# Kernel tuning notes

Measured on AMD Instinct MI355X. Metric: run time of the kernel, lower is better.

The kernel has to match this reference:

```python
import jax, jax.numpy as jnp
import numpy as np
from jax import lax

# Dimensions (see shape_source)
B, J, I, E, H = 256, 128, 64, 512, 512   # batch, target len, source len, embed, hidden
MAXJW = 128                               # max jump width
WJ = 2 * MAXJW + 1                        # size of jump-width set (257)
ALPHA_P0 = 1.0
EPS = 1e-29


def setup_inputs() -> dict:
    key = jax.random.key(0)
    ks = jax.random.split(key, 10)
    return {
        "y_hidden": jax.random.normal(ks[0], (B, J, E), jnp.float32),
        "y_hidden_null": jax.random.normal(ks[1], (1, 1, E), jnp.float32),
        "W_trans": jax.random.normal(ks[2], (E, H), jnp.float32) * 0.02,
        "b_trans": jnp.zeros((H,), jnp.float32),
        "W_jump": jax.random.normal(ks[3], (H, WJ), jnp.float32) * 0.02,
        "b_jump": jnp.zeros((WJ,), jnp.float32),
        "W_p0": jax.random.normal(ks[4], (H, 1), jnp.float32) * 0.02,
        "b_p0": jnp.zeros((1,), jnp.float32),
        # emission probs p(source_t | target_state_k), kept near 1 to avoid
        # underflow of the unrescaled HMM forward product (as in original).
        "emission": jax.random.uniform(ks[5], (B, 2 * J, I), jnp.float32) * 0.5 + 0.75,
        "source_lengths": jax.random.randint(ks[6], (B,), 1, I + 1, dtype=jnp.int32),
        "target_lengths": jax.random.randint(ks[7], (B,), 1, J + 1, dtype=jnp.int32),
    }


def _build_transition(y_hidden, y_hidden_null, W_trans, b_trans, W_jump, b_jump, W_p0, b_p0):
    # get_transition: Dense(tanh) -> Dense(softmax) jump widths; Dense(sigmoid) p0.
    ts = jnp.tanh(y_hidden @ W_trans + b_trans)           # [B,J,H]
    ts_null = jnp.tanh(y_hidden_null @ W_trans + b_trans) # [1,1,H]
    jump_prob = jax.nn.softmax(ts @ W_jump + b_jump, axis=-1)  # [B,J,WJ]
    p0_scalar = ALPHA_P0 * jax.nn.sigmoid(ts_null @ W_p0 + b_p0)[0, 0, 0]
    p0 = jnp.broadcast_to(p0_scalar, (y_hidden.shape[0], J))  # tile to [B,J]
    # gather jump widths: row i takes jump_prob[:, i, MAXJW + k - i] for k in [0,J)
    idx = MAXJW + jnp.arange(J)[None, :] - jnp.arange(J)[:, None]        # [J,J]
    idxb = jnp.broadcast_to(idx[None], (jump_prob.shape[0], J, J))
    jw = jnp.take_along_axis(jump_prob, idxb, axis=2)                    # [B,J,J]
    jw = jw * (1.0 - p0[:, :, None]) / jnp.sum(jw, axis=2, keepdims=True)
    diag_p0 = p0[:, :, None] * jnp.eye(J, dtype=jw.dtype)                # [B,J,J]
    T_half = jnp.concatenate([jw, diag_p0], axis=2)                      # [B,J,2J]
    return jnp.concatenate([T_half, T_half], axis=1)                     # [B,2J,2J]


def reference(y_hidden, y_hidden_null, W_trans, b_trans, W_jump, b_jump,
              W_p0, b_p0, emission, source_lengths, target_lengths):
    T = _build_transition(y_hidden, y_hidden_null, W_trans, b_trans,
                          W_jump, b_jump, W_p0, b_p0)       # [B,2J,2J]
    e = jnp.transpose(emission, (2, 0, 1))                  # [I,B,2J]
    # tf.scan with no initializer: f_0 = emission at source position 0
    f0 = e[0]

    def step(f, et):
        f_next = jnp.einsum('bj,bjk->bk', f, T) * et        # forward recursion
        return f_next, f_next

    _, fs = lax.scan(step, f0, e[1:])
    fs = jnp.concatenate([f0[None], fs], axis=0)            # [I,B,2J]
    fbt = jnp.transpose(fs, (1, 2, 0))                      # [B,2J,I]
    last_idx = (source_lengths - 1).astype(jnp.int32)[:, None, None]
    last = jnp.take_along_axis(fbt, last_idx, axis=2)[:, :, 0]  # [B,2J]
    m = (jnp.arange(J)[None, :] < target_lengths[:, None]).astype(last.dtype)
    mask = jnp.concatenate([m, m], axis=1)                  # [B,2J]
    return jnp.log(jnp.sum(last * mask, axis=1) + EPS)      # [B]
```

## Files before the change

kernel.cpp:

```cpp
#include <hip/hip_runtime.h>
#include <stdint.h>

typedef __attribute__((ext_vector_type(8))) short bf16x8;
typedef __attribute__((ext_vector_type(4))) float f32x4;

__device__ __forceinline__ unsigned short f2bf(float f) {
  union { float f; unsigned int u; } un; un.f = f;
  unsigned int r = un.u + 0x7fffu + ((un.u >> 16) & 1u);
  return (unsigned short)(r >> 16);
}

__device__ __forceinline__ float tanh_fast(float x) {
  x = fminf(15.f, fmaxf(-15.f, x));
  float e = __expf(2.f * x);
  return (e - 1.f) / (e + 1.f);
}

__device__ __forceinline__ void gload_lds16(const void* g, void* l) {
  __builtin_amdgcn_global_load_lds(
      (const __attribute__((address_space(1))) unsigned int*)(unsigned long long)g,
      (__attribute__((address_space(3))) unsigned int*)(unsigned int)(unsigned long long)l,
      16, 0, 0);
}

__global__ __launch_bounds__(256) void cvt_y_kernel(
    const float* __restrict__ x, unsigned short* __restrict__ y, int n4) {
  int i = blockIdx.x * blockDim.x + threadIdx.x;
  if (i < n4) {
    const float4 v = reinterpret_cast<const float4*>(x)[i];
    ushort4 o;
    o.x = f2bf(v.x); o.y = f2bf(v.y); o.z = f2bf(v.z); o.w = f2bf(v.w);
    reinterpret_cast<ushort4*>(y)[i] = o;
  }
}

__global__ __launch_bounds__(256) void cvt_transpose_kernel(
    const float* __restrict__ W, unsigned short* __restrict__ Wt,
    int R, int C, int ldW) {
  int i = blockIdx.x * blockDim.x + threadIdx.x;
  if (i < R * C) {
    int c = i / R, r = i - c * R;
    Wt[(size_t)c * R + r] = f2bf(W[(size_t)r * ldW + c]);
  }
}

__global__ __launch_bounds__(512) void p0_kernel(
    const float* __restrict__ ynull, const float* __restrict__ W_trans,
    const float* __restrict__ b_trans, const float* __restrict__ W_p0,
    const float* __restrict__ b_p0, float* __restrict__ p0buf) {
  __shared__ float red[512];
  const int hh = threadIdx.x;
  float acc = 0.f;
  for (int e = 0; e < 512; ++e) acc = fmaf(ynull[e], W_trans[(size_t)e * 512 + hh], acc);
  const float ts = tanhf(acc + b_trans[hh]);
  red[hh] = ts * W_p0[hh];
  __syncthreads();
  for (int s = 256; s > 0; s >>= 1) {
    if (hh < s) red[hh] += red[hh + s];
    __syncthreads();
  }
  if (hh == 0) {
    const float z = red[0] + b_p0[0];
    const float p0 = 1.f / (1.f + __expf(-z));
    p0buf[0] = p0;
    p0buf[1] = 1.f - p0;
  }
}

template <int EPI>
__global__ __launch_bounds__(256, 2) void gemm_tt(
    const unsigned short* __restrict__ A, const unsigned short* __restrict__ Bt,
    const float* __restrict__ bias, void* __restrict__ Cout,
    int M, int N, int K) {
  __shared__ unsigned short sA[128 * 32];
  __shared__ unsigned short sB[128 * 32];
  const int tid = threadIdx.x;
  const int lane = tid & 63;
  const int wave = tid >> 6;
  const int wr = wave >> 1, wc = wave & 1;
  const int m0 = blockIdx.x * 128, n0 = blockIdx.y * 128;

  f32x4 acc[4][4] = {};

  const int srow = lane >> 2;
  const int scol = (lane & 3) * 8;
  const int c0 = wave * 2, c1 = wave * 2 + 1;
  const unsigned short* Ar0 = A + (size_t)(m0 + c0 * 16 + srow) * K + scol;
  const unsigned short* Ar1 = A + (size_t)(m0 + c1 * 16 + srow) * K + scol;
  const unsigned short* Br0 = Bt + (size_t)(n0 + c0 * 16 + srow) * K + scol;
  const unsigned short* Br1 = Bt + (size_t)(n0 + c1 * 16 + srow) * K + scol;

  for (int kk = 0; kk < K; kk += 32) {
    __syncthreads();
    gload_lds16(Ar0 + kk, &sA[c0 * 512]);
    gload_lds16(Ar1 + kk, &sA[c1 * 512]);
    gload_lds16(Br0 + kk, &sB[c0 * 512]);
    gload_lds16(Br1 + kk, &sB[c1 * 512]);
    __syncthreads();
    bf16x8 af[4], bfr[4];
#pragma unroll
    for (int mi = 0; mi < 4; ++mi)
      af[mi] = *reinterpret_cast<const bf16x8*>(
          &sA[(wr * 64 + mi * 16 + (lane & 15)) * 32 + (lane >> 4) * 8]);
#pragma unroll
    for (int ni = 0; ni < 4; ++ni)
      bfr[ni] = *reinterpret_cast<const bf16x8*>(
          &sB[(wc * 64 + ni * 16 + (lane & 15)) * 32 + (lane >> 4) * 8]);
#pragma unroll
    for (int mi = 0; mi < 4; ++mi)
#pragma unroll
      for (int ni = 0; ni < 4; ++ni)
        acc[mi][ni] = __builtin_amdgcn_mfma_f32_16x16x32_bf16(
            af[mi], bfr[ni], acc[mi][ni], 0, 0, 0);
  }

  const int crow0 = m0 + wr * 64 + (lane >> 4) * 4;
  const int ccol0 = n0 + wc * 64 + (lane & 15);
#pragma unroll
  for (int mi = 0; mi < 4; ++mi) {
#pragma unroll
    for (int ni = 0; ni < 4; ++ni) {
      const int gcol = ccol0 + ni * 16;
      const float bv = bias[gcol];
#pragma unroll
      for (int r = 0; r < 4; ++r) {
        const int grow = crow0 + mi * 16 + r;
        const float v = acc[mi][ni][r] + bv;
        if constexpr (EPI == 0) {
          ((unsigned short*)Cout)[(size_t)grow * N + gcol] = f2bf(tanh_fast(v));
        } else {
          ((float*)Cout)[(size_t)grow * N + gcol] = v;
        }
      }
    }
  }
}

__global__ __launch_bounds__(256) void wsoftmax_kernel(
    const float* __restrict__ logits, const float* __restrict__ p0buf,
    float* __restrict__ jwout) {
  const int lane = threadIdx.x & 63;
  const int wave = threadIdx.x >> 6;
  const int row = blockIdx.x * 4 + wave;
  const int i = row & 127;
  const float* lrow = logits + (size_t)row * 256 + (128 - i);
  const float v0 = lrow[lane];
  const float v1 = lrow[lane + 64];
  float mx = fmaxf(v0, v1);
#pragma unroll
  for (int off = 32; off > 0; off >>= 1) mx = fmaxf(mx, __shfl_xor(mx, off));
  const float e0 = __expf(v0 - mx);
  const float e1 = __expf(v1 - mx);
  float s = e0 + e1;
#pragma unroll
  for (int off = 32; off > 0; off >>= 1) s += __shfl_xor(s, off);
  const float scale = p0buf[1] / s;
  float* orow = jwout + (size_t)row * 128;
  orow[lane] = e0 * scale;
  orow[lane + 64] = e1 * scale;
}

__global__ __launch_bounds__(256, 1) void forward_hmm(
    const float* __restrict__ jw, const float* __restrict__ emission,
    const float* __restrict__ p0buf, const int* __restrict__ slen_p,
    const int* __restrict__ tlen_p, float* __restrict__ out) {
  __shared__ float gbuf[2][128];
  __shared__ float part[2][128];
  __shared__ float red[4];
  const int b = blockIdx.x;
  const int tid = threadIdx.x;
  const int k = tid & 127;
  const int h = tid >> 7;
  const int lane = tid & 63;
  const int wave = tid >> 6;

  const float* eb = emission + (size_t)b * 256 * 64;

  float jwreg[64];
  {
    const float* jb = jw + (size_t)b * 16384 + (size_t)(h * 64) * 128 + k;
#pragma unroll
    for (int j = 0; j < 64; ++j) jwreg[j] = jb[(size_t)j * 128];
  }
  const float p0 = p0buf[0];
  const int S = slen_p[b];
  const int T = tlen_p[b];

  if (h == 0) gbuf[0][k] = eb[k * 64] + eb[(128 + k) * 64];
  __syncthreads();

  const int steps = S - 1;
  int cur = 0;
  for (int t = 1; t <= steps; ++t) {
    float e0 = 0.f, e1 = 0.f;
    if (h == 0) {
      e0 = eb[k * 64 + t];
      e1 = eb[(128 + k) * 64 + t];
    }
    float acc = 0.f;
    const float* gv = &gbuf[cur][h * 64];
#pragma unroll
    for (int c = 0; c < 16; ++c) {
      const float4 g4 = *reinterpret_cast<const float4*>(&gv[c * 4]);
      acc = fmaf(g4.x, jwreg[c * 4 + 0], acc);
      acc = fmaf(g4.y, jwreg[c * 4 + 1], acc);
      acc = fmaf(g4.z, jwreg[c * 4 + 2], acc);
      acc = fmaf(g4.w, jwreg[c * 4 + 3], acc);
    }
    part[h][k] = acc;
    __syncthreads();
    if (h == 0) {
      const float s = part[0][k] + part[1][k];
      gbuf[cur ^ 1][k] = fmaf(s, e0, gbuf[cur][k] * p0 * e1);
    }
    __syncthreads();
    cur ^= 1;
  }

  float val = 0.f;
  if (h == 0 && k < T) val = gbuf[cur][k];
#pragma unroll
  for (int off = 32; off > 0; off >>= 1) val += __shfl_xor(val, off);
  if (lane == 0) red[wave] = val;
  __syncthreads();
  if (tid == 0) out[b] = logf(red[0] + red[1] + red[2] + red[3] + 1e-29f);
}

extern "C" void kernel_launch(void* const* d_in, const int* in_sizes, int n_in,
                              void* d_out, int out_size, void* d_ws, size_t ws_size,
                              hipStream_t stream) {
  const float* y_hidden = (const float*)d_in[0];
  const float* y_null   = (const float*)d_in[1];
  const float* W_trans  = (const float*)d_in[2];
  const float* b_trans  = (const float*)d_in[3];
  const float* W_jump   = (const float*)d_in[4];
  const float* b_jump   = (const float*)d_in[5];
  const float* W_p0     = (const float*)d_in[6];
  const float* b_p0     = (const float*)d_in[7];
  const float* emission = (const float*)d_in[8];
  const int* slen = (const int*)d_in[9];
  const int* tlen = (const int*)d_in[10];
  float* out = (float*)d_out;

  char* ws = (char*)d_ws;
  unsigned short* a16   = (unsigned short*)ws;
  float* logits         = (float*)ws;
  unsigned short* ts16  = (unsigned short*)(ws + 33554432);
  unsigned short* wt16t = (unsigned short*)(ws + 67108864);
  unsigned short* wj16t = (unsigned short*)(ws + 67633152);
  float* p0buf          = (float*)(ws + 67895296);
  float* jwbuf          = (float*)(ws + 67895552);

  cvt_y_kernel<<<dim3(16384), dim3(256), 0, stream>>>(y_hidden, a16, 16777216 / 4);
  cvt_transpose_kernel<<<dim3((512 * 512 + 255) / 256), dim3(256), 0, stream>>>(
      W_trans, wt16t, 512, 512, 512);
  cvt_transpose_kernel<<<dim3((512 * 256 + 255) / 256), dim3(256), 0, stream>>>(
      W_jump, wj16t, 512, 256, 257);
  p0_kernel<<<dim3(1), dim3(512), 0, stream>>>(y_null, W_trans, b_trans, W_p0, b_p0, p0buf);

  gemm_tt<0><<<dim3(256, 4), dim3(256), 0, stream>>>(a16, wt16t, b_trans, (void*)ts16,
                                                     32768, 512, 512);
  gemm_tt<1><<<dim3(256, 2), dim3(256), 0, stream>>>(ts16, wj16t, b_jump, (void*)logits,
                                                     32768, 256, 512);
  wsoftmax_kernel<<<dim3(8192), dim3(256), 0, stream>>>(logits, p0buf, jwbuf);
  forward_hmm<<<dim3(256), dim3(256), 0, stream>>>(jwbuf, emission, p0buf, slen, tlen, out);
}
```

Baseline: 135.7 us.

## Run HMM forward recursion on MFMA with bf16 transition in a single wave

```diff
diff --git a/kernel.cpp b/kernel.cpp
--- a/kernel.cpp
+++ b/kernel.cpp
@@ -14,6 +14,12 @@
   x = fminf(15.f, fmaxf(-15.f, x));
   float e = __expf(2.f * x);
   return (e - 1.f) / (e + 1.f);
+}
+
+__device__ __forceinline__ unsigned int cvt_pk_bf16(float lo, float hi) {
+  unsigned int r;
+  asm("v_cvt_pk_bf16_f32 %0, %1, %2" : "=v"(r) : "v"(lo), "v"(hi));
+  return r;
 }
 
 __device__ __forceinline__ void gload_lds16(const void* g, void* l) {
@@ -138,7 +144,7 @@
 
 __global__ __launch_bounds__(256) void wsoftmax_kernel(
     const float* __restrict__ logits, const float* __restrict__ p0buf,
-    float* __restrict__ jwout) {
+    unsigned short* __restrict__ jwout) {
   const int lane = threadIdx.x & 63;
   const int wave = threadIdx.x >> 6;
   const int row = blockIdx.x * 4 + wave;
@@ -155,75 +161,98 @@
 #pragma unroll
   for (int off = 32; off > 0; off >>= 1) s += __shfl_xor(s, off);
   const float scale = p0buf[1] / s;
-  float* orow = jwout + (size_t)row * 128;
-  orow[lane] = e0 * scale;
-  orow[lane + 64] = e1 * scale;
-}
-
-__global__ __launch_bounds__(256, 1) void forward_hmm(
-    const float* __restrict__ jw, const float* __restrict__ emission,
+  unsigned short* orow = jwout + (size_t)row * 128;
+  orow[lane] = f2bf(e0 * scale);
+  orow[lane + 64] = f2bf(e1 * scale);
+}
+
+__global__ __launch_bounds__(64, 1) void forward_hmm_mfma(
+    const unsigned short* __restrict__ jwb,
+    const float* __restrict__ emission,
     const float* __restrict__ p0buf, const int* __restrict__ slen_p,
     const int* __restrict__ tlen_p, float* __restrict__ out) {
-  __shared__ float gbuf[2][128];
-  __shared__ float part[2][128];
-  __shared__ float red[4];
+  __shared__ float gl[128];
   const int b = blockIdx.x;
-  const int tid = threadIdx.x;
-  const int k = tid & 127;
-  const int h = tid >> 7;
-  const int lane = tid & 63;
-  const int wave = tid >> 6;
-
-  const float* eb = emission + (size_t)b * 256 * 64;
-
-  float jwreg[64];
-  {
-    const float* jb = jw + (size_t)b * 16384 + (size_t)(h * 64) * 128 + k;
-#pragma unroll
-    for (int j = 0; j < 64; ++j) jwreg[j] = jb[(size_t)j * 128];
-  }
+  const int l = threadIdx.x;
+  const int m = l & 15;
+  const int q = l >> 4;
+
+  const unsigned short* jwt = jwb + (size_t)b * 16384;
+  bf16x8 bfr[4][8];
+#pragma unroll
+  for (int kt = 0; kt < 4; ++kt) {
+    const int r0 = kt * 32 + q * 8;
+#pragma unroll
+    for (int nt = 0; nt < 8; ++nt) {
+      const int c = nt * 16 + m;
+      bf16x8 v;
+#pragma unroll
+      for (int j = 0; j < 8; ++j) v[j] = (short)jwt[(size_t)(r0 + j) * 128 + c];
+      bfr[kt][nt] = v;
+    }
+  }
+
   const float p0 = p0buf[0];
   const int S = slen_p[b];
   const int T = tlen_p[b];
-
-  if (h == 0) gbuf[0][k] = eb[k * 64] + eb[(128 + k) * 64];
-  __syncthreads();
-
-  const int steps = S - 1;
-  int cur = 0;
-  for (int t = 1; t <= steps; ++t) {
-    float e0 = 0.f, e1 = 0.f;
-    if (h == 0) {
-      e0 = eb[k * 64 + t];
-      e1 = eb[(128 + k) * 64 + t];
-    }
-    float acc = 0.f;
-    const float* gv = &gbuf[cur][h * 64];
-#pragma unroll
-    for (int c = 0; c < 16; ++c) {
-      const float4 g4 = *reinterpret_cast<const float4*>(&gv[c * 4]);
-      acc = fmaf(g4.x, jwreg[c * 4 + 0], acc);
-      acc = fmaf(g4.y, jwreg[c * 4 + 1], acc);
-      acc = fmaf(g4.z, jwreg[c * 4 + 2], acc);
-      acc = fmaf(g4.w, jwreg[c * 4 + 3], acc);
-    }
-    part[h][k] = acc;
-    __syncthreads();
-    if (h == 0) {
-      const float s = part[0][k] + part[1][k];
-      gbuf[cur ^ 1][k] = fmaf(s, e0, gbuf[cur][k] * p0 * e1);
-    }
-    __syncthreads();
-    cur ^= 1;
+  const float* eb = emission + (size_t)b * 16384;
+
+  float gown[8];
+#pragma unroll
+  for (int nt = 0; nt < 8; ++nt) {
+    const int k = nt * 16 + m;
+    gown[nt] = eb[(size_t)k * 64] + eb[(size_t)(k + 128) * 64];
+  }
+  if (q == 0) {
+#pragma unroll
+    for (int nt = 0; nt < 8; ++nt) gl[nt * 16 + m] = gown[nt];
+  }
+
+  for (int t = 1; t < S; ++t) {
+    float e0[8], e1[8];
+#pragma unroll
+    for (int nt = 0; nt < 8; ++nt) {
+      const int k = nt * 16 + m;
+      e0[nt] = eb[(size_t)k * 64 + t];
+      e1[nt] = eb[(size_t)(k + 128) * 64 + t];
+    }
+    bf16x8 af[4];
+#pragma unroll
+    for (int kt = 0; kt < 4; ++kt) {
+      const float4 lo = *reinterpret_cast<const float4*>(&gl[kt * 32 + q * 8]);
+      const float4 hi = *reinterpret_cast<const float4*>(&gl[kt * 32 + q * 8 + 4]);
+      union { unsigned int u[4]; bf16x8 v; } pk;
+      pk.u[0] = cvt_pk_bf16(lo.x, lo.y);
+      pk.u[1] = cvt_pk_bf16(lo.z, lo.w);
+      pk.u[2] = cvt_pk_bf16(hi.x, hi.y);
+      pk.u[3] = cvt_pk_bf16(hi.z, hi.w);
+      af[kt] = pk.v;
+    }
+    f32x4 acc[8];
+#pragma unroll
+    for (int nt = 0; nt < 8; ++nt) {
+      f32x4 a = __builtin_amdgcn_mfma_f32_16x16x32_bf16(
+          af[0], bfr[0][nt], (f32x4){0.f, 0.f, 0.f, 0.f}, 0, 0, 0);
+      a = __builtin_amdgcn_mfma_f32_16x16x32_bf16(af[1], bfr[1][nt], a, 0, 0, 0);
+      a = __builtin_amdgcn_mfma_f32_16x16x32_bf16(af[2], bfr[2][nt], a, 0, 0, 0);
+      acc[nt] = __builtin_amdgcn_mfma_f32_16x16x32_bf16(af[3], bfr[3][nt], a, 0, 0, 0);
+    }
+#pragma unroll
+    for (int nt = 0; nt < 8; ++nt)
+      gown[nt] = fmaf(acc[nt][0], e0[nt], gown[nt] * (p0 * e1[nt]));
+    if (q == 0) {
+#pragma unroll
+      for (int nt = 0; nt < 8; ++nt) gl[nt * 16 + m] = gown[nt];
+    }
   }
 
   float val = 0.f;
-  if (h == 0 && k < T) val = gbuf[cur][k];
-#pragma unroll
-  for (int off = 32; off > 0; off >>= 1) val += __shfl_xor(val, off);
-  if (lane == 0) red[wave] = val;
-  __syncthreads();
-  if (tid == 0) out[b] = logf(red[0] + red[1] + red[2] + red[3] + 1e-29f);
+#pragma unroll
+  for (int nt = 0; nt < 8; ++nt)
+    if (nt * 16 + m < T) val += gown[nt];
+#pragma unroll
+  for (int off = 1; off < 16; off <<= 1) val += __shfl_xor(val, off);
+  if (l == 0) out[b] = logf(val + 1e-29f);
 }
 
 extern "C" void kernel_launch(void* const* d_in, const int* in_sizes, int n_in,
@@ -249,7 +278,7 @@
   unsigned short* wt16t = (unsigned short*)(ws + 67108864);
   unsigned short* wj16t = (unsigned short*)(ws + 67633152);
   float* p0buf          = (float*)(ws + 67895296);
-  float* jwbuf          = (float*)(ws + 67895552);
+  unsigned short* jwb16 = (unsigned short*)(ws + 67895552);
 
   cvt_y_kernel<<<dim3(16384), dim3(256), 0, stream>>>(y_hidden, a16, 16777216 / 4);
   cvt_transpose_kernel<<<dim3((512 * 512 + 255) / 256), dim3(256), 0, stream>>>(
@@ -262,6 +291,7 @@
                                                      32768, 512, 512);
   gemm_tt<1><<<dim3(256, 2), dim3(256), 0, stream>>>(ts16, wj16t, b_jump, (void*)logits,
                                                      32768, 256, 512);
-  wsoftmax_kernel<<<dim3(8192), dim3(256), 0, stream>>>(logits, p0buf, jwbuf);
-  forward_hmm<<<dim3(256), dim3(256), 0, stream>>>(jwbuf, emission, p0buf, slen, tlen, out);
-}
+  wsoftmax_kernel<<<dim3(8192), dim3(256), 0, stream>>>(logits, p0buf, jwb16);
+  forward_hmm_mfma<<<dim3(256), dim3(64), 0, stream>>>(jwb16, emission, p0buf,
+                                                       slen, tlen, out);
+}
```

Result: slower. 146.6 us (+8.1%).
